# Performance work log

Hardware: AMD Instinct MI355X
Metric: run time of the kernel (lower is better)

The kernel has to match this reference:

```python
import jax, jax.numpy as jnp
import numpy as np

EMBED_DIM = 1024
NUM_HEADS = 16
EFF_HEADS = NUM_HEADS // 2
HEAD_DIM = EMBED_DIM // NUM_HEADS
LAMBDA_INIT = 0.8
B, N = 2, 2048


def setup_inputs() -> dict:
    key = jax.random.key(0)
    ks = jax.random.split(key, 14)
    s = 0.02
    return {
        "x": jax.random.normal(ks[0], (B, N, EMBED_DIM), dtype=jnp.float32),
        "Wq": jax.random.normal(ks[1], (EMBED_DIM, EMBED_DIM), dtype=jnp.float32) * s,
        "bq": jnp.zeros((EMBED_DIM,), dtype=jnp.float32),
        "Wk": jax.random.normal(ks[2], (EMBED_DIM, EMBED_DIM), dtype=jnp.float32) * s,
        "bk": jnp.zeros((EMBED_DIM,), dtype=jnp.float32),
        "Wv": jax.random.normal(ks[3], (EMBED_DIM, EMBED_DIM), dtype=jnp.float32) * s,
        "bv": jnp.zeros((EMBED_DIM,), dtype=jnp.float32),
        "Wp": jax.random.normal(ks[4], (EMBED_DIM, EMBED_DIM), dtype=jnp.float32) * s,
        "bp": jnp.zeros((EMBED_DIM,), dtype=jnp.float32),
        "lambda_q1": jax.random.normal(ks[5], (EFF_HEADS, 1, HEAD_DIM), dtype=jnp.float32) * s,
        "lambda_k1": jax.random.normal(ks[6], (EFF_HEADS, 1, HEAD_DIM), dtype=jnp.float32) * s,
        "lambda_q2": jax.random.normal(ks[7], (EFF_HEADS, 1, HEAD_DIM), dtype=jnp.float32) * s,
        "lambda_k2": jax.random.normal(ks[8], (EFF_HEADS, 1, HEAD_DIM), dtype=jnp.float32) * s,
    }


def reference(x, Wq, bq, Wk, bk, Wv, bv, Wp, bp,
              lambda_q1, lambda_k1, lambda_q2, lambda_k2):
    Bb, Nn, C = x.shape
    H, H2, hd = NUM_HEADS, EFF_HEADS, HEAD_DIM
    scale = hd ** (-0.5)

    # projections (torch Linear: y = x @ W.T + b), reshape to [B,H,N,hd]
    q = (x @ Wq.T + bq).reshape(Bb, Nn, H, hd).transpose(0, 2, 1, 3)
    k = (x @ Wk.T + bk).reshape(Bb, Nn, H, hd).transpose(0, 2, 1, 3)
    v = (x @ Wv.T + bv).reshape(Bb, Nn, H, hd).transpose(0, 2, 1, 3)

    q1, q2 = q[:, :H2], q[:, H2:]
    k1, k2 = k[:, :H2], k[:, H2:]
    v1, v2 = v[:, :H2], v[:, H2:]

    # scalar lambda: per-head dot products, clamped exp, differenced, averaged
    l1 = jnp.exp(jnp.minimum((lambda_q1 * lambda_k1).sum((-1, -2)), 5.0))  # [H2]
    l2 = jnp.exp(jnp.minimum((lambda_q2 * lambda_k2).sum((-1, -2)), 5.0))
    lv = (l1 - l2 + LAMBDA_INIT).mean()

    a1 = jax.nn.softmax(jnp.einsum('bhnd,bhmd->bhnm', q1, k1) * scale, axis=-1)
    x1 = jnp.einsum('bhnm,bhmd->bhnd', a1, v1).transpose(0, 2, 1, 3).reshape(Bb, Nn, C // 2)
    a2 = jax.nn.softmax(jnp.einsum('bhnd,bhmd->bhnm', q2, k2) * scale, axis=-1)
    x2 = jnp.einsum('bhnm,bhmd->bhnd', a2, v2).transpose(0, 2, 1, 3).reshape(Bb, Nn, C // 2)

    out = jnp.concatenate([x1 - lv * x2, x2], axis=-1) @ Wp.T + bp
    return out
```

## Files before the change

kernel.cpp:

```cpp
#include <hip/hip_runtime.h>

typedef __bf16 bf16;
typedef __bf16 bf16x8 __attribute__((ext_vector_type(8)));
typedef __bf16 bf16x4 __attribute__((ext_vector_type(4)));
typedef float  f32x16 __attribute__((ext_vector_type(16)));
typedef unsigned int uint;
typedef unsigned int uintx4 __attribute__((ext_vector_type(4)));

#define QSCALE (0.125f * 1.44269504088896340736f)

__device__ __forceinline__ void g2l16(const void* g, void* l) {
  __builtin_amdgcn_global_load_lds(
      (const __attribute__((address_space(1))) void*)g,
      (__attribute__((address_space(3))) void*)l, 16, 0, 0);
}

__device__ __forceinline__ f32x16 mfma16(bf16x8 a, bf16x8 b, f32x16 c) {
  return __builtin_amdgcn_mfma_f32_32x32x16_bf16(a, b, c, 0, 0, 0);
}


__global__ void cast5_kernel(const float* __restrict__ x,
                             const float* __restrict__ wq, const float* __restrict__ wk,
                             const float* __restrict__ wv, const float* __restrict__ wp,
                             const float* __restrict__ lq1, const float* __restrict__ lk1,
                             const float* __restrict__ lq2, const float* __restrict__ lk2,
                             bf16* __restrict__ xb, bf16* __restrict__ wqkv,
                             bf16* __restrict__ wpb) {
  int bx = blockIdx.x;
  int seg, idx;
  if (bx < 2048) { seg = 0; idx = bx; }
  else { int t = bx - 2048; seg = 1 + (t >> 9); idx = t & 511; }
  long i = (long)(idx * 256 + threadIdx.x) * 8;
  const float* s; bf16* d;
  if (seg == 0)      { s = x;  d = xb; }
  else if (seg == 1) { s = wq; d = wqkv; }
  else if (seg == 2) { s = wk; d = wqkv + 1048576; }
  else if (seg == 3) { s = wv; d = wqkv + 2097152; }
  else               { s = wp; d = wpb; }
  float4 f0 = *(const float4*)(s + i);
  float4 f1 = *(const float4*)(s + i + 4);
  if (seg == 4 && (i & 1023) >= 512) {
    int t = threadIdx.x & 63;
    float accum = 0.f;
    for (int hh = 0; hh < 8; ++hh) {
      float v1 = lq1[hh*64 + t] * lk1[hh*64 + t];
      float v2 = lq2[hh*64 + t] * lk2[hh*64 + t];
      for (int off = 32; off; off >>= 1) {
        v1 += __shfl_xor(v1, off);
        v2 += __shfl_xor(v2, off);
      }
      accum += expf(fminf(v1, 5.f)) - expf(fminf(v2, 5.f));
    }
    float lv = accum / 8.f + 0.8f;
    float4 g0 = *(const float4*)(s + i - 512);
    float4 g1 = *(const float4*)(s + i - 508);
    f0.x -= lv * g0.x; f0.y -= lv * g0.y; f0.z -= lv * g0.z; f0.w -= lv * g0.w;
    f1.x -= lv * g1.x; f1.y -= lv * g1.y; f1.z -= lv * g1.z; f1.w -= lv * g1.w;
  }
  bf16x8 o;
  o[0] = (bf16)f0.x; o[1] = (bf16)f0.y; o[2] = (bf16)f0.z; o[3] = (bf16)f0.w;
  o[4] = (bf16)f1.x; o[5] = (bf16)f1.y; o[6] = (bf16)f1.z; o[7] = (bf16)f1.w;
  *(bf16x8*)(d + i) = o;
}

__global__ __launch_bounds__(256, 2) void gemm_qkv_kernel(
    const bf16* __restrict__ A, const bf16* __restrict__ B,
    const float* __restrict__ bias0, const float* __restrict__ bias1,
    const float* __restrict__ bias2,
    bf16* __restrict__ O0, bf16* __restrict__ O1, bf16* __restrict__ O2) {
  __shared__ __align__(16) char smem[34 * 1024];
  const int tid = threadIdx.x;
  const int w = tid >> 6, L = tid & 63;
  const int l31 = L & 31, h5 = L >> 5;
  const int m0 = blockIdx.x * 128;
  const int n0g = blockIdx.y * 128;
  const int by = n0g >> 10;
  const bf16* Bp = B + (long)by * 1048576;
  const float* biasp = (by == 0) ? bias0 : ((by == 1) ? bias1 : bias2);
  const int nloc = n0g & 1023;

  f32x16 acc[2][2];
  for (int i = 0; i < 2; ++i) for (int j = 0; j < 2; ++j)
    for (int r = 0; r < 16; ++r) acc[i][j][r] = 0.f;

  const int srow = L >> 1, spar = L & 1;
  const int wm = w >> 1, wn = w & 1;
  const int fs = (l31 * 2 + h5) * 16;

  for (int k0 = 0; k0 < 1024; k0 += 64) {
    for (int i = 0; i < 8; ++i) {
      int r = w * 8 + i;
      int rr = r & 15;
      int rowblk = rr >> 2, kst = rr & 3;
      int row = rowblk * 32 + srow;
      int kk = k0 + (kst * 2 + spar) * 8;
      const bf16* gsrc = (r < 16) ? (A + (long)(m0 + row) * 1024 + kk)
                                  : (Bp + (long)(nloc + row) * 1024 + kk);
      g2l16(gsrc, smem + r * 1024);
    }
    __syncthreads();
    for (int kst = 0; kst < 4; ++kst) {
      bf16x8 a0 = *(const bf16x8*)(smem + (((wm * 2 + 0) * 4 + kst) * 1024) + fs);
      bf16x8 a1 = *(const bf16x8*)(smem + (((wm * 2 + 1) * 4 + kst) * 1024) + fs);
      bf16x8 b0 = *(const bf16x8*)(smem + 16384 + (((wn * 2 + 0) * 4 + kst) * 1024) + fs);
      bf16x8 b1 = *(const bf16x8*)(smem + 16384 + (((wn * 2 + 1) * 4 + kst) * 1024) + fs);
      acc[0][0] = mfma16(a0, b0, acc[0][0]);
      acc[0][1] = mfma16(a0, b1, acc[0][1]);
      acc[1][0] = mfma16(a1, b0, acc[1][0]);
      acc[1][1] = mfma16(a1, b1, acc[1][1]);
    }
    __syncthreads();
  }

  if (by == 2) {
    bf16* vt = (bf16*)smem;
    int b = m0 >> 11;
    int nbase = (m0 & 2047);
    for (int mi = 0; mi < 2; ++mi) for (int ni = 0; ni < 2; ++ni) {
      int lcol = wn * 64 + ni * 32 + l31;
      float bias_v = biasp[nloc + lcol];
      for (int g = 0; g < 4; ++g) {
        bf16x4 pk;
        for (int r = 0; r < 4; ++r) pk[r] = (bf16)(acc[mi][ni][g * 4 + r] + bias_v);
        int Qp = mi * 4 + g;
        int lslot = wm * 64 + (Qp >> 1) * 16 + h5 * 8 + (Qp & 1) * 4;
        *(bf16x4*)(vt + lcol * 132 + lslot) = pk;
      }
    }
    __syncthreads();
    for (int rr = 0; rr < 32; ++rr) {
      int lcol = w * 32 + rr;
      int col = nloc + lcol;
      int hh = col >> 6, d = col & 63;
      uint val = *(const uint*)(vt + lcol * 132 + L * 2);
      *(uint*)(O2 + ((long)(b * 16 + hh) * 64 + d) * 2048 + nbase + L * 2) = val;
    }
  } else {
    bf16* dst = (by == 0) ? O0 : O1;
    float scale = (by == 0) ? QSCALE : 1.0f;
    for (int mi = 0; mi < 2; ++mi) for (int ni = 0; ni < 2; ++ni) {
      int col = nloc + wn * 64 + ni * 32 + l31;
      float bias_v = biasp[col];
      int row_base = m0 + wm * 64 + mi * 32 + 4 * h5;
      for (int reg = 0; reg < 16; ++reg) {
        int rowoff = (reg & 3) + 8 * (reg >> 2);
        float v = (acc[mi][ni][reg] + bias_v) * scale;
        dst[(long)(row_base + rowoff) * 1024 + col] = (bf16)v;
      }
    }
  }
}

__global__ __launch_bounds__(256, 2) void gemm_proj_kernel(
    const bf16* __restrict__ A, const bf16* __restrict__ B,
    const float* __restrict__ bias, float* __restrict__ Of) {
  __shared__ __align__(16) char smem[32 * 1024];
  const int tid = threadIdx.x;
  const int w = tid >> 6, L = tid & 63;
  const int l31 = L & 31, h5 = L >> 5;
  const int m0 = blockIdx.x * 128;
  const int n0 = blockIdx.y * 128;

  f32x16 acc[2][2];
  for (int i = 0; i < 2; ++i) for (int j = 0; j < 2; ++j)
    for (int r = 0; r < 16; ++r) acc[i][j][r] = 0.f;

  const int srow = L >> 1, spar = L & 1;
  const int wm = w >> 1, wn = w & 1;
  const int fs = (l31 * 2 + h5) * 16;

  for (int k0 = 0; k0 < 1024; k0 += 64) {
    for (int i = 0; i < 8; ++i) {
      int r = w * 8 + i;
      int rr = r & 15;
      int rowblk = rr >> 2, kst = rr & 3;
      int row = rowblk * 32 + srow;
      int kk = k0 + (kst * 2 + spar) * 8;
      const bf16* gsrc = (r < 16) ? (A + (long)(m0 + row) * 1024 + kk)
                                  : (B + (long)(n0 + row) * 1024 + kk);
      g2l16(gsrc, smem + r * 1024);
    }
    __syncthreads();
    for (int kst = 0; kst < 4; ++kst) {
      bf16x8 a0 = *(const bf16x8*)(smem + (((wm * 2 + 0) * 4 + kst) * 1024) + fs);
      bf16x8 a1 = *(const bf16x8*)(smem + (((wm * 2 + 1) * 4 + kst) * 1024) + fs);
      bf16x8 b0 = *(const bf16x8*)(smem + 16384 + (((wn * 2 + 0) * 4 + kst) * 1024) + fs);
      bf16x8 b1 = *(const bf16x8*)(smem + 16384 + (((wn * 2 + 1) * 4 + kst) * 1024) + fs);
      acc[0][0] = mfma16(a0, b0, acc[0][0]);
      acc[0][1] = mfma16(a0, b1, acc[0][1]);
      acc[1][0] = mfma16(a1, b0, acc[1][0]);
      acc[1][1] = mfma16(a1, b1, acc[1][1]);
    }
    __syncthreads();
  }

  for (int mi = 0; mi < 2; ++mi) for (int ni = 0; ni < 2; ++ni) {
    int col = n0 + wn * 64 + ni * 32 + l31;
    float bias_v = bias[col];
    int row_base = m0 + wm * 64 + mi * 32 + 4 * h5;
    for (int reg = 0; reg < 16; ++reg) {
      int rowoff = (reg & 3) + 8 * (reg >> 2);
      Of[(long)(row_base + rowoff) * 1024 + col] = acc[mi][ni][reg] + bias_v;
    }
  }
}

__global__ __launch_bounds__(512, 4) void attn_kernel(
    const bf16* __restrict__ Qb, const bf16* __restrict__ Kb,
    const bf16* __restrict__ Vt, bf16* __restrict__ Ob) {
  __shared__ __align__(16) char smem[65536];
  const int tid = threadIdx.x, w = tid >> 6, L = tid & 63;
  const int half = w >> 2, pair = w & 3;
  const int bh = blockIdx.x, qt = blockIdx.y;
  const int b = bh >> 4, h = bh & 15;
  const int q0 = qt * 128 + pair * 32;
  const int l31 = L & 31, h5 = L >> 5;
  const int srow = L >> 1, spar = L & 1;
  const int fs = (l31 * 2 + h5) * 16;

  bf16x8 qf[4];
  for (int kst = 0; kst < 4; ++kst)
    qf[kst] = *(const bf16x8*)(Qb + (long)(b * 2048 + q0 + l31) * 1024 + h * 64
                               + kst * 16 + h5 * 8);

  f32x16 o[2];
  for (int i = 0; i < 2; ++i)
    for (int r = 0; r < 16; ++r) o[i][r] = 0.f;
  float ls[4] = {0.f, 0.f, 0.f, 0.f};

  const bf16* Kbh = Kb + (long)b * 2048 * 1024 + h * 64 + (long)half * 1024 * 1024;
  const bf16* Vth = Vt + (long)bh * 64 * 2048 + half * 1024;

  char* kb0 = smem + half * 16384;
  char* kb1 = smem + 32768 + half * 16384;

  auto stage = [&](int t, char* kb) {
    int n0 = t * 64;
    for (int i = 0; i < 4; ++i) {
      int r = pair * 4 + i;
      if (r < 8) {
        int nkb = r >> 2, kst = r & 3;
        const bf16* g = Kbh + (long)(n0 + nkb * 32 + srow) * 1024 + (kst * 2 + spar) * 8;
        g2l16(g, kb + r * 1024);
      } else {
        int rr = r - 8, db = rr >> 2, kst = rr & 3;
        const bf16* g = Vth + (long)(db * 32 + srow) * 2048 + n0 + (kst * 2 + spar) * 8;
        g2l16(g, kb + 8192 + rr * 1024);
      }
    }
  };

  stage(0, kb0);
  stage(1, kb1);

  for (int t = 0; t < 16; ++t) {
    char* kb = (t & 1) ? kb1 : kb0;
    if (t < 15) asm volatile("s_waitcnt vmcnt(4)" ::: "memory");
    else        asm volatile("s_waitcnt vmcnt(0)" ::: "memory");
    __builtin_amdgcn_s_barrier();

    f32x16 s[2];
    {
      bf16x8 k0f = *(const bf16x8*)(kb + fs);
      bf16x8 k1f = *(const bf16x8*)(kb + 4 * 1024 + fs);
      f32x16 z = {};
      __builtin_amdgcn_s_setprio(1);
      s[0] = mfma16(k0f, qf[0], z);
      s[1] = mfma16(k1f, qf[0], z);
      __builtin_amdgcn_s_setprio(0);
    }
    for (int kst = 1; kst < 4; ++kst) {
      bf16x8 k0f = *(const bf16x8*)(kb + (kst * 1024) + fs);
      bf16x8 k1f = *(const bf16x8*)(kb + ((4 + kst) * 1024) + fs);
      __builtin_amdgcn_s_setprio(1);
      s[0] = mfma16(k0f, qf[kst], s[0]);
      s[1] = mfma16(k1f, qf[kst], s[1]);
      __builtin_amdgcn_s_setprio(0);
    }

    for (int nki = 0; nki < 2; ++nki)
      for (int r = 0; r < 16; ++r) {
        float p = __builtin_amdgcn_exp2f(s[nki][r]);
        s[nki][r] = p;
        ls[r & 3] += p;
      }

    for (int kst = 0; kst < 4; ++kst) {
      bf16x8 v0 = *(const bf16x8*)(kb + 8192 + (kst * 1024) + fs);
      bf16x8 v1 = *(const bf16x8*)(kb + 8192 + ((4 + kst) * 1024) + fs);
      int nki = kst >> 1;
      int rbase = (kst & 1) * 8;
      bf16x8 pf;
#pragma unroll
      for (int j = 0; j < 8; ++j) pf[j] = (bf16)s[nki][rbase + j];
      __builtin_amdgcn_s_setprio(1);
      o[0] = mfma16(v0, pf, o[0]);
      o[1] = mfma16(v1, pf, o[1]);
      __builtin_amdgcn_s_setprio(0);
    }

    __builtin_amdgcn_s_barrier();
    if (t + 2 < 16) stage(t + 2, kb);
  }

  float lsum = (ls[0] + ls[1]) + (ls[2] + ls[3]);
  float lcol = lsum + __shfl_xor(lsum, 32);
  if (half) {
    float* dstO = (float*)smem + pair * 2112;
    for (int di = 0; di < 2; ++di)
      for (int r = 0; r < 16; ++r) dstO[L * 33 + di * 16 + r] = o[di][r];
    if (h5 == 0) ((float*)(smem + 33792))[pair * 32 + l31] = lcol;
  }
  __syncthreads();
  float linv = 0.f;
  if (!half) {
    float* srcO = (float*)smem + pair * 2112;
    for (int di = 0; di < 2; ++di)
      for (int r = 0; r < 16; ++r) o[di][r] += srcO[L * 33 + di * 16 + r];
    float lother = ((float*)(smem + 33792))[pair * 32 + l31];
    linv = 1.f / (lcol + lother);
  }
  __syncthreads();
  if (!half) {
    char* ot = smem + pair * 4352;
    for (int di = 0; di < 2; ++di)
      for (int g = 0; g < 4; ++g) {
        bf16x4 pk;
        for (int r = 0; r < 4; ++r)
          pk[r] = (bf16)(o[di][g * 4 + r] * linv);
        int d0 = di * 32 + g * 8 + h5 * 4;
        *(bf16x4*)(ot + (l31 * 68 + d0) * 2) = pk;
      }
    for (int i = 0; i < 4; ++i) {
      int qloc = (L >> 3) + i * 8;
      int cc = L & 7;
      bf16x8 vv = *(const bf16x8*)(ot + (qloc * 68 + cc * 8) * 2);
      *(bf16x8*)(Ob + (long)(b * 2048 + q0 + qloc) * 1024 + h * 64 + cc * 8) = vv;
    }
  }
}

extern "C" void kernel_launch(void* const* d_in, const int* in_sizes, int n_in,
                              void* d_out, int out_size, void* d_ws, size_t ws_size,
                              hipStream_t stream) {
  const float* x   = (const float*)d_in[0];
  const float* Wq  = (const float*)d_in[1];
  const float* bq  = (const float*)d_in[2];
  const float* Wk  = (const float*)d_in[3];
  const float* bk  = (const float*)d_in[4];
  const float* Wv  = (const float*)d_in[5];
  const float* bv  = (const float*)d_in[6];
  const float* Wp  = (const float*)d_in[7];
  const float* bp  = (const float*)d_in[8];
  const float* lq1 = (const float*)d_in[9];
  const float* lk1 = (const float*)d_in[10];
  const float* lq2 = (const float*)d_in[11];
  const float* lk2 = (const float*)d_in[12];
  float* out = (float*)d_out;

  char* ws = (char*)d_ws;
  bf16* xb   = (bf16*)(ws + 1024);
  bf16* Wqkv = xb + (long)4096 * 1024;
  bf16* Wpb  = Wqkv + (long)3 * 1024 * 1024;
  bf16* Vt   = Wpb + (long)1024 * 1024;
  bf16* Ob   = Vt + (long)4096 * 1024;
  bf16* Qb = (bf16*)d_out;
  bf16* Kb = Qb + (long)4096 * 1024;

  cast5_kernel<<<dim3(4096), 256, 0, stream>>>(
      x, Wq, Wk, Wv, Wp, lq1, lk1, lq2, lk2, xb, Wqkv, Wpb);
  gemm_qkv_kernel<<<dim3(32, 24), 256, 0, stream>>>(
      xb, Wqkv, bq, bk, bv, Qb, Kb, Vt);
  attn_kernel<<<dim3(32, 16), 512, 0, stream>>>(Qb, Kb, Vt, Ob);
  gemm_proj_kernel<<<dim3(32, 8), 256, 0, stream>>>(Ob, Wpb, bp, out);
}
```

Measured before the change: 204.1 us.

## Shrink attention blocks to 256 threads with single-buffered split K/V staging

The attention kernel drops from 512 to 256 threads per block, with 64 query rows per block and twice as many blocks. LDS use is halved by replacing double-buffering with a single buffer per half: one wave loads the next K tile while the current tile's V is consumed, and the other wave loads the next V tile after PV. This is meant to raise occupancy and the number of blocks across CUs. In exchange it adds more barriers per iteration and less prefetch distance, which may expose load latency, and K/V are re-read by twice as many blocks.

```diff
diff --git a/kernel.cpp b/kernel.cpp
--- a/kernel.cpp
+++ b/kernel.cpp
@@ -206,15 +206,15 @@
   }
 }
 
-__global__ __launch_bounds__(512, 4) void attn_kernel(
+__global__ __launch_bounds__(256, 4) void attn_kernel(
     const bf16* __restrict__ Qb, const bf16* __restrict__ Kb,
     const bf16* __restrict__ Vt, bf16* __restrict__ Ob) {
-  __shared__ __align__(16) char smem[65536];
+  __shared__ __align__(16) char smem[32768];
   const int tid = threadIdx.x, w = tid >> 6, L = tid & 63;
-  const int half = w >> 2, pair = w & 3;
+  const int half = w >> 1, pair = w & 1;
   const int bh = blockIdx.x, qt = blockIdx.y;
   const int b = bh >> 4, h = bh & 15;
-  const int q0 = qt * 128 + pair * 32;
+  const int q0 = qt * 64 + pair * 32;
   const int l31 = L & 31, h5 = L >> 5;
   const int srow = L >> 1, spar = L & 1;
   const int fs = (l31 * 2 + h5) * 16;
@@ -232,38 +232,36 @@
   const bf16* Kbh = Kb + (long)b * 2048 * 1024 + h * 64 + (long)half * 1024 * 1024;
   const bf16* Vth = Vt + (long)bh * 64 * 2048 + half * 1024;
 
-  char* kb0 = smem + half * 16384;
-  char* kb1 = smem + 32768 + half * 16384;
-
-  auto stage = [&](int t, char* kb) {
+  char* kbase = smem + half * 16384;
+
+  auto stageK = [&](int t) {
     int n0 = t * 64;
-    for (int i = 0; i < 4; ++i) {
-      int r = pair * 4 + i;
-      if (r < 8) {
-        int nkb = r >> 2, kst = r & 3;
-        const bf16* g = Kbh + (long)(n0 + nkb * 32 + srow) * 1024 + (kst * 2 + spar) * 8;
-        g2l16(g, kb + r * 1024);
-      } else {
-        int rr = r - 8, db = rr >> 2, kst = rr & 3;
-        const bf16* g = Vth + (long)(db * 32 + srow) * 2048 + n0 + (kst * 2 + spar) * 8;
-        g2l16(g, kb + 8192 + rr * 1024);
-      }
+    for (int r = 0; r < 8; ++r) {
+      const bf16* g = Kbh + (long)(n0 + (r >> 2) * 32 + srow) * 1024
+                      + ((r & 3) * 2 + spar) * 8;
+      g2l16(g, kbase + r * 1024);
     }
   };
-
-  stage(0, kb0);
-  stage(1, kb1);
+  auto stageV = [&](int t) {
+    int n0 = t * 64;
+    for (int rr = 0; rr < 8; ++rr) {
+      const bf16* g = Vth + (long)((rr >> 2) * 32 + srow) * 2048 + n0
+                      + ((rr & 3) * 2 + spar) * 8;
+      g2l16(g, kbase + 8192 + rr * 1024);
+    }
+  };
+
+  if (pair == 0) stageK(0); else stageV(0);
 
   for (int t = 0; t < 16; ++t) {
-    char* kb = (t & 1) ? kb1 : kb0;
-    if (t < 15) asm volatile("s_waitcnt vmcnt(4)" ::: "memory");
-    else        asm volatile("s_waitcnt vmcnt(0)" ::: "memory");
+    if (pair == 0) asm volatile("s_waitcnt vmcnt(0)" ::: "memory");
     __builtin_amdgcn_s_barrier();
+    __builtin_amdgcn_sched_barrier(0);
 
     f32x16 s[2];
     {
-      bf16x8 k0f = *(const bf16x8*)(kb + fs);
-      bf16x8 k1f = *(const bf16x8*)(kb + 4 * 1024 + fs);
+      bf16x8 k0f = *(const bf16x8*)(kbase + fs);
+      bf16x8 k1f = *(const bf16x8*)(kbase + 4 * 1024 + fs);
       f32x16 z = {};
       __builtin_amdgcn_s_setprio(1);
       s[0] = mfma16(k0f, qf[0], z);
@@ -271,13 +269,16 @@
       __builtin_amdgcn_s_setprio(0);
     }
     for (int kst = 1; kst < 4; ++kst) {
-      bf16x8 k0f = *(const bf16x8*)(kb + (kst * 1024) + fs);
-      bf16x8 k1f = *(const bf16x8*)(kb + ((4 + kst) * 1024) + fs);
+      bf16x8 k0f = *(const bf16x8*)(kbase + (kst * 1024) + fs);
+      bf16x8 k1f = *(const bf16x8*)(kbase + ((4 + kst) * 1024) + fs);
       __builtin_amdgcn_s_setprio(1);
       s[0] = mfma16(k0f, qf[kst], s[0]);
       s[1] = mfma16(k1f, qf[kst], s[1]);
       __builtin_amdgcn_s_setprio(0);
     }
+
+    __builtin_amdgcn_s_barrier();
+    if (pair == 0 && t + 1 < 16) stageK(t + 1);
 
     for (int nki = 0; nki < 2; ++nki)
       for (int r = 0; r < 16; ++r) {
@@ -286,9 +287,13 @@
         ls[r & 3] += p;
       }
 
+    if (pair == 1) asm volatile("s_waitcnt vmcnt(0)" ::: "memory");
+    __builtin_amdgcn_s_barrier();
+    __builtin_amdgcn_sched_barrier(0);
+
     for (int kst = 0; kst < 4; ++kst) {
-      bf16x8 v0 = *(const bf16x8*)(kb + 8192 + (kst * 1024) + fs);
-      bf16x8 v1 = *(const bf16x8*)(kb + 8192 + ((4 + kst) * 1024) + fs);
+      bf16x8 v0 = *(const bf16x8*)(kbase + 8192 + (kst * 1024) + fs);
+      bf16x8 v1 = *(const bf16x8*)(kbase + 8192 + ((4 + kst) * 1024) + fs);
       int nki = kst >> 1;
       int rbase = (kst & 1) * 8;
       bf16x8 pf;
@@ -301,7 +306,7 @@
     }
 
     __builtin_amdgcn_s_barrier();
-    if (t + 2 < 16) stage(t + 2, kb);
+    if (pair == 1 && t + 1 < 16) stageV(t + 1);
   }
 
   float lsum = (ls[0] + ls[1]) + (ls[2] + ls[3]);
@@ -310,7 +315,7 @@
     float* dstO = (float*)smem + pair * 2112;
     for (int di = 0; di < 2; ++di)
       for (int r = 0; r < 16; ++r) dstO[L * 33 + di * 16 + r] = o[di][r];
-    if (h5 == 0) ((float*)(smem + 33792))[pair * 32 + l31] = lcol;
+    if (h5 == 0) ((float*)(smem + 16896))[pair * 32 + l31] = lcol;
   }
   __syncthreads();
   float linv = 0.f;
@@ -318,7 +323,7 @@
     float* srcO = (float*)smem + pair * 2112;
     for (int di = 0; di < 2; ++di)
       for (int r = 0; r < 16; ++r) o[di][r] += srcO[L * 33 + di * 16 + r];
-    float lother = ((float*)(smem + 33792))[pair * 32 + l31];
+    float lother = ((float*)(smem + 16896))[pair * 32 + l31];
     linv = 1.f / (lcol + lother);
   }
   __syncthreads();
@@ -372,6 +377,6 @@
       x, Wq, Wk, Wv, Wp, lq1, lk1, lq2, lk2, xb, Wqkv, Wpb);
   gemm_qkv_kernel<<<dim3(32, 24), 256, 0, stream>>>(
       xb, Wqkv, bq, bk, bv, Qb, Kb, Vt);
-  attn_kernel<<<dim3(32, 16), 512, 0, stream>>>(Qb, Kb, Vt, Ob);
+  attn_kernel<<<dim3(32, 32), 256, 0, stream>>>(Qb, Kb, Vt, Ob);
   gemm_proj_kernel<<<dim3(32, 8), 256, 0, stream>>>(Ob, Wpb, bp, out);
 }
```

Measured after the change: 209.8 us. 1.03x slower.

## Process two 32-row query tiles per wave in attention, halving block threads

Applied to the files above, without the earlier changes.

The attention kernel now uses 256 threads (4 waves) instead of 512. Each wave handles 64 query rows as two 32-row tiles that share every K and V fragment read from LDS. Staging is split so one wave loads K and the other loads V, each issuing 8 global-to-LDS loads, with the vmcnt wait adjusted to match. This cuts LDS reads per MFMA and the number of waves, at the cost of doubled accumulator registers and fewer waves to hide latency.

```diff
diff --git a/kernel.cpp b/kernel.cpp
--- a/kernel.cpp
+++ b/kernel.cpp
@@ -206,28 +206,31 @@
   }
 }
 
-__global__ __launch_bounds__(512, 4) void attn_kernel(
+__global__ __launch_bounds__(256, 2) void attn_kernel(
     const bf16* __restrict__ Qb, const bf16* __restrict__ Kb,
     const bf16* __restrict__ Vt, bf16* __restrict__ Ob) {
   __shared__ __align__(16) char smem[65536];
   const int tid = threadIdx.x, w = tid >> 6, L = tid & 63;
-  const int half = w >> 2, pair = w & 3;
+  const int half = w >> 1, sub = w & 1;
   const int bh = blockIdx.x, qt = blockIdx.y;
   const int b = bh >> 4, h = bh & 15;
-  const int q0 = qt * 128 + pair * 32;
+  const int q0 = qt * 128 + sub * 64;
   const int l31 = L & 31, h5 = L >> 5;
   const int srow = L >> 1, spar = L & 1;
   const int fs = (l31 * 2 + h5) * 16;
 
-  bf16x8 qf[4];
-  for (int kst = 0; kst < 4; ++kst)
-    qf[kst] = *(const bf16x8*)(Qb + (long)(b * 2048 + q0 + l31) * 1024 + h * 64
-                               + kst * 16 + h5 * 8);
-
-  f32x16 o[2];
+  bf16x8 qfA[4], qfB[4];
+  for (int kst = 0; kst < 4; ++kst) {
+    long qoff = (long)(b * 2048 + q0 + l31) * 1024 + h * 64 + kst * 16 + h5 * 8;
+    qfA[kst] = *(const bf16x8*)(Qb + qoff);
+    qfB[kst] = *(const bf16x8*)(Qb + qoff + 32 * 1024);
+  }
+
+  f32x16 oA[2], oB[2];
   for (int i = 0; i < 2; ++i)
-    for (int r = 0; r < 16; ++r) o[i][r] = 0.f;
-  float ls[4] = {0.f, 0.f, 0.f, 0.f};
+    for (int r = 0; r < 16; ++r) { oA[i][r] = 0.f; oB[i][r] = 0.f; }
+  float lsA[4] = {0.f, 0.f, 0.f, 0.f};
+  float lsB[4] = {0.f, 0.f, 0.f, 0.f};
 
   const bf16* Kbh = Kb + (long)b * 2048 * 1024 + h * 64 + (long)half * 1024 * 1024;
   const bf16* Vth = Vt + (long)bh * 64 * 2048 + half * 1024;
@@ -237,14 +240,15 @@
 
   auto stage = [&](int t, char* kb) {
     int n0 = t * 64;
-    for (int i = 0; i < 4; ++i) {
-      int r = pair * 4 + i;
-      if (r < 8) {
+    if (sub == 0) {
+      for (int r = 0; r < 8; ++r) {
         int nkb = r >> 2, kst = r & 3;
         const bf16* g = Kbh + (long)(n0 + nkb * 32 + srow) * 1024 + (kst * 2 + spar) * 8;
         g2l16(g, kb + r * 1024);
-      } else {
-        int rr = r - 8, db = rr >> 2, kst = rr & 3;
+      }
+    } else {
+      for (int rr = 0; rr < 8; ++rr) {
+        int db = rr >> 2, kst = rr & 3;
         const bf16* g = Vth + (long)(db * 32 + srow) * 2048 + n0 + (kst * 2 + spar) * 8;
         g2l16(g, kb + 8192 + rr * 1024);
       }
@@ -256,47 +260,58 @@
 
   for (int t = 0; t < 16; ++t) {
     char* kb = (t & 1) ? kb1 : kb0;
-    if (t < 15) asm volatile("s_waitcnt vmcnt(4)" ::: "memory");
+    if (t < 15) asm volatile("s_waitcnt vmcnt(8)" ::: "memory");
     else        asm volatile("s_waitcnt vmcnt(0)" ::: "memory");
     __builtin_amdgcn_s_barrier();
 
-    f32x16 s[2];
+    f32x16 sA0, sA1, sB0, sB1;
     {
       bf16x8 k0f = *(const bf16x8*)(kb + fs);
       bf16x8 k1f = *(const bf16x8*)(kb + 4 * 1024 + fs);
       f32x16 z = {};
       __builtin_amdgcn_s_setprio(1);
-      s[0] = mfma16(k0f, qf[0], z);
-      s[1] = mfma16(k1f, qf[0], z);
+      sA0 = mfma16(k0f, qfA[0], z);
+      sA1 = mfma16(k1f, qfA[0], z);
+      sB0 = mfma16(k0f, qfB[0], z);
+      sB1 = mfma16(k1f, qfB[0], z);
       __builtin_amdgcn_s_setprio(0);
     }
+#pragma unroll
     for (int kst = 1; kst < 4; ++kst) {
       bf16x8 k0f = *(const bf16x8*)(kb + (kst * 1024) + fs);
       bf16x8 k1f = *(const bf16x8*)(kb + ((4 + kst) * 1024) + fs);
       __builtin_amdgcn_s_setprio(1);
-      s[0] = mfma16(k0f, qf[kst], s[0]);
-      s[1] = mfma16(k1f, qf[kst], s[1]);
+      sA0 = mfma16(k0f, qfA[kst], sA0);
+      sA1 = mfma16(k1f, qfA[kst], sA1);
+      sB0 = mfma16(k0f, qfB[kst], sB0);
+      sB1 = mfma16(k1f, qfB[kst], sB1);
       __builtin_amdgcn_s_setprio(0);
     }
 
-    for (int nki = 0; nki < 2; ++nki)
-      for (int r = 0; r < 16; ++r) {
-        float p = __builtin_amdgcn_exp2f(s[nki][r]);
-        s[nki][r] = p;
-        ls[r & 3] += p;
-      }
-
+#pragma unroll
+    for (int r = 0; r < 16; ++r) {
+      float p0 = __builtin_amdgcn_exp2f(sA0[r]); sA0[r] = p0; lsA[r & 3] += p0;
+      float p1 = __builtin_amdgcn_exp2f(sA1[r]); sA1[r] = p1; lsA[r & 3] += p1;
+      float p2 = __builtin_amdgcn_exp2f(sB0[r]); sB0[r] = p2; lsB[r & 3] += p2;
+      float p3 = __builtin_amdgcn_exp2f(sB1[r]); sB1[r] = p3; lsB[r & 3] += p3;
+    }
+
+#pragma unroll
     for (int kst = 0; kst < 4; ++kst) {
       bf16x8 v0 = *(const bf16x8*)(kb + 8192 + (kst * 1024) + fs);
       bf16x8 v1 = *(const bf16x8*)(kb + 8192 + ((4 + kst) * 1024) + fs);
-      int nki = kst >> 1;
       int rbase = (kst & 1) * 8;
-      bf16x8 pf;
+      bf16x8 pfA, pfB;
 #pragma unroll
-      for (int j = 0; j < 8; ++j) pf[j] = (bf16)s[nki][rbase + j];
+      for (int j = 0; j < 8; ++j) {
+        pfA[j] = (bf16)((kst < 2) ? sA0[rbase + j] : sA1[rbase + j]);
+        pfB[j] = (bf16)((kst < 2) ? sB0[rbase + j] : sB1[rbase + j]);
+      }
       __builtin_amdgcn_s_setprio(1);
-      o[0] = mfma16(v0, pf, o[0]);
-      o[1] = mfma16(v1, pf, o[1]);
+      oA[0] = mfma16(v0, pfA, oA[0]);
+      oA[1] = mfma16(v1, pfA, oA[1]);
+      oB[0] = mfma16(v0, pfB, oB[0]);
+      oB[1] = mfma16(v1, pfB, oB[1]);
       __builtin_amdgcn_s_setprio(0);
     }
 
@@ -304,39 +319,60 @@
     if (t + 2 < 16) stage(t + 2, kb);
   }
 
-  float lsum = (ls[0] + ls[1]) + (ls[2] + ls[3]);
-  float lcol = lsum + __shfl_xor(lsum, 32);
+  float lA = (lsA[0] + lsA[1]) + (lsA[2] + lsA[3]);
+  float lB = (lsB[0] + lsB[1]) + (lsB[2] + lsB[3]);
+  float lcolA = lA + __shfl_xor(lA, 32);
+  float lcolB = lB + __shfl_xor(lB, 32);
   if (half) {
-    float* dstO = (float*)smem + pair * 2112;
+    float* dstA = (float*)smem + (sub * 2 + 0) * 2112;
+    float* dstB = (float*)smem + (sub * 2 + 1) * 2112;
     for (int di = 0; di < 2; ++di)
-      for (int r = 0; r < 16; ++r) dstO[L * 33 + di * 16 + r] = o[di][r];
-    if (h5 == 0) ((float*)(smem + 33792))[pair * 32 + l31] = lcol;
+      for (int r = 0; r < 16; ++r) {
+        dstA[L * 33 + di * 16 + r] = oA[di][r];
+        dstB[L * 33 + di * 16 + r] = oB[di][r];
+      }
+    if (h5 == 0) {
+      ((float*)(smem + 33792))[(sub * 2 + 0) * 32 + l31] = lcolA;
+      ((float*)(smem + 33792))[(sub * 2 + 1) * 32 + l31] = lcolB;
+    }
   }
   __syncthreads();
-  float linv = 0.f;
+  float linvA = 0.f, linvB = 0.f;
   if (!half) {
-    float* srcO = (float*)smem + pair * 2112;
+    float* srcA = (float*)smem + (sub * 2 + 0) * 2112;
+    float* srcB = (float*)smem + (sub * 2 + 1) * 2112;
     for (int di = 0; di < 2; ++di)
-      for (int r = 0; r < 16; ++r) o[di][r] += srcO[L * 33 + di * 16 + r];
-    float lother = ((float*)(smem + 33792))[pair * 32 + l31];
-    linv = 1.f / (lcol + lother);
+      for (int r = 0; r < 16; ++r) {
+        oA[di][r] += srcA[L * 33 + di * 16 + r];
+        oB[di][r] += srcB[L * 33 + di * 16 + r];
+      }
+    float loA = ((float*)(smem + 33792))[(sub * 2 + 0) * 32 + l31];
+    float loB = ((float*)(smem + 33792))[(sub * 2 + 1) * 32 + l31];
+    linvA = 1.f / (lcolA + loA);
+    linvB = 1.f / (lcolB + loB);
   }
   __syncthreads();
   if (!half) {
-    char* ot = smem + pair * 4352;
+    char* otA = smem + (sub * 2 + 0) * 4352;
+    char* otB = smem + (sub * 2 + 1) * 4352;
     for (int di = 0; di < 2; ++di)
       for (int g = 0; g < 4; ++g) {
-        bf16x4 pk;
-        for (int r = 0; r < 4; ++r)
-          pk[r] = (bf16)(o[di][g * 4 + r] * linv);
+        bf16x4 pkA, pkB;
+        for (int r = 0; r < 4; ++r) {
+          pkA[r] = (bf16)(oA[di][g * 4 + r] * linvA);
+          pkB[r] = (bf16)(oB[di][g * 4 + r] * linvB);
+        }
         int d0 = di * 32 + g * 8 + h5 * 4;
-        *(bf16x4*)(ot + (l31 * 68 + d0) * 2) = pk;
+        *(bf16x4*)(otA + (l31 * 68 + d0) * 2) = pkA;
+        *(bf16x4*)(otB + (l31 * 68 + d0) * 2) = pkB;
       }
     for (int i = 0; i < 4; ++i) {
       int qloc = (L >> 3) + i * 8;
       int cc = L & 7;
-      bf16x8 vv = *(const bf16x8*)(ot + (qloc * 68 + cc * 8) * 2);
-      *(bf16x8*)(Ob + (long)(b * 2048 + q0 + qloc) * 1024 + h * 64 + cc * 8) = vv;
+      bf16x8 vA = *(const bf16x8*)(otA + (qloc * 68 + cc * 8) * 2);
+      bf16x8 vB = *(const bf16x8*)(otB + (qloc * 68 + cc * 8) * 2);
+      *(bf16x8*)(Ob + (long)(b * 2048 + q0 + qloc) * 1024 + h * 64 + cc * 8) = vA;
+      *(bf16x8*)(Ob + (long)(b * 2048 + q0 + 32 + qloc) * 1024 + h * 64 + cc * 8) = vB;
     }
   }
 }
@@ -372,6 +408,6 @@
       x, Wq, Wk, Wv, Wp, lq1, lk1, lq2, lk2, xb, Wqkv, Wpb);
   gemm_qkv_kernel<<<dim3(32, 24), 256, 0, stream>>>(
       xb, Wqkv, bq, bk, bv, Qb, Kb, Vt);
-  attn_kernel<<<dim3(32, 16), 512, 0, stream>>>(Qb, Kb, Vt, Ob);
+  attn_kernel<<<dim3(32, 16), 256, 0, stream>>>(Qb, Kb, Vt, Ob);
   gemm_proj_kernel<<<dim3(32, 8), 256, 0, stream>>>(Ob, Wpb, bp, out);
 }
```

After: 204.5 us. No clear change (+0.2%).
